# Optimization experiments

Hardware: AMD Instinct MI355X
Metric: run time of the kernel (lower is better)

The kernel has to match this reference:

```python
import jax, jax.numpy as jnp
import numpy as np

DIM = 2048
NUM_HEADS = 16
NUM_KV_HEADS = 4
HEAD_DIM = DIM // NUM_HEADS  # 128
ROPE_DIMS = HEAD_DIM         # rope_dims=0 -> full head_dim
ROPE_BASE = 10000.0
EPS = jnp.finfo(jnp.float32).eps  # torch F.rms_norm default eps


def _rms_norm(x):
    # F.rms_norm over last dim, no learned weight
    return x * jax.lax.rsqrt(jnp.mean(x * x, axis=-1, keepdims=True) + EPS)


def _rope_cos_sin(seq_len, dtype):
    inv_freq = 1.0 / (ROPE_BASE ** (jnp.arange(0, ROPE_DIMS, 2, dtype=jnp.float32) / ROPE_DIMS))
    t = jnp.arange(seq_len, dtype=jnp.float32)
    freqs = jnp.outer(t, inv_freq)  # [S, rope_dims/2]
    return jnp.cos(freqs).astype(dtype), jnp.sin(freqs).astype(dtype)


def _apply_rotary(x, cos, sin):
    # x: [B, H, S, hd]; cos/sin: [S, rope_dims/2] broadcast over B,H
    half = ROPE_DIMS // 2
    x1, x2 = x[..., :half], x[..., half:ROPE_DIMS]
    x_pass = x[..., ROPE_DIMS:]
    rotated = jnp.concatenate((x1 * cos + x2 * sin, -x1 * sin + x2 * cos), axis=-1)
    return jnp.concatenate((rotated, x_pass), axis=-1) if x_pass.shape[-1] else rotated


def setup_inputs() -> dict:
    key = jax.random.key(0)
    ks = jax.random.split(key, 6)
    B, S = 2, 2048
    kv_dim = NUM_KV_HEADS * HEAD_DIM
    scale = 0.02
    return {
        "x": jax.random.normal(ks[0], (B, S, DIM), dtype=jnp.float32),
        "Wq": jax.random.normal(ks[1], (DIM, DIM), dtype=jnp.float32) * scale,
        "Wk": jax.random.normal(ks[2], (kv_dim, DIM), dtype=jnp.float32) * scale,
        "Wv": jax.random.normal(ks[3], (kv_dim, DIM), dtype=jnp.float32) * scale,
        "Wproj": jax.random.normal(ks[4], (DIM, DIM), dtype=jnp.float32) * scale,
        "q_gain": jnp.full((NUM_HEADS,), 1.0, dtype=jnp.float32),
    }


def reference(x, Wq, Wk, Wv, Wproj, q_gain):
    B, S, D = x.shape
    H, KV, hd = NUM_HEADS, NUM_KV_HEADS, HEAD_DIM
    group = H // KV

    # QKV projections (Linear: y = x @ W.T)
    q = (x @ Wq.T).reshape(B, S, H, hd).transpose(0, 2, 1, 3)    # [B,H,S,hd]
    k = (x @ Wk.T).reshape(B, S, KV, hd).transpose(0, 2, 1, 3)   # [B,KV,S,hd]
    v = (x @ Wv.T).reshape(B, S, KV, hd).transpose(0, 2, 1, 3)

    # Per-head RMSNorm on q/k
    q = _rms_norm(q)
    k = _rms_norm(k)

    # RoPE
    cos, sin = _rope_cos_sin(S, q.dtype)
    q = _apply_rotary(q, cos, sin)
    k = _apply_rotary(k, cos, sin)

    # Per-head gain on q
    q = q * q_gain[None, :, None, None]

    # GQA: expand kv heads to H
    k = jnp.repeat(k, group, axis=1)  # [B,H,S,hd]
    v = jnp.repeat(v, group, axis=1)

    # Causal SDPA
    sm_scale = 1.0 / np.sqrt(hd)
    scores = jnp.einsum('bhqd,bhkd->bhqk', q, k) * sm_scale
    causal = jnp.tril(jnp.ones((S, S), dtype=bool))
    scores = jnp.where(causal, scores, -jnp.inf)
    attn = jax.nn.softmax(scores, axis=-1)
    y = jnp.einsum('bhqk,bhkd->bhqd', attn, v)

    y = y.transpose(0, 2, 1, 3).reshape(B, S, D)
    return y @ Wproj.T
```

## Files before the change

kernel.cpp:

```cpp
#include <hip/hip_runtime.h>
#include <hip/hip_bf16.h>
#include <stdint.h>

namespace {

constexpr int kB = 2;
constexpr int kS = 2048;
constexpr int kD = 2048;
constexpr int kH = 16;
constexpr int kKV = 4;
constexpr int kHd = 128;
constexpr int kM = kB * kS;
constexpr int kQKN = kD + kKV * kHd;

using bf = __bf16;
typedef bf bf16x8 __attribute__((ext_vector_type(8)));
typedef float f32x4 __attribute__((ext_vector_type(4)));
typedef float f32x16 __attribute__((ext_vector_type(16)));

__device__ __forceinline__ f32x4 mfma16(bf16x8 a, bf16x8 b, f32x4 c) {
  return __builtin_amdgcn_mfma_f32_16x16x32_bf16(a, b, c, 0, 0, 0);
}
__device__ __forceinline__ f32x16 mfma32(bf16x8 a, bf16x8 b, f32x16 c) {
  return __builtin_amdgcn_mfma_f32_32x32x16_bf16(a, b, c, 0, 0, 0);
}

__device__ __forceinline__ void gload_lds16(const bf* g, bf* l) {
  __builtin_amdgcn_global_load_lds(
      (const __attribute__((address_space(1))) void*)(uintptr_t)g,
      (__attribute__((address_space(3))) void*)l, 16, 0, 0);
}

__global__ __launch_bounds__(256) void cvt_kernel(const float* __restrict__ src,
                                                  bf* __restrict__ dst, int n4) {
  int i = blockIdx.x * 256 + threadIdx.x;
  if (i >= n4) return;
  float4 v = reinterpret_cast<const float4*>(src)[i];
  union { bf h[4]; uint2 u; } o;
  o.h[0] = (bf)v.x; o.h[1] = (bf)v.y; o.h[2] = (bf)v.z; o.h[3] = (bf)v.w;
  reinterpret_cast<uint2*>(dst)[i] = o.u;
}

template <typename CT>
__global__ __launch_bounds__(256) void gemm_bt(const bf* __restrict__ A, int lda,
                                               const bf* __restrict__ Bm, int ldb,
                                               CT* __restrict__ C, int ldc, int K) {
  __shared__ bf As[128 * 64];
  __shared__ bf Bs[128 * 64];
  const int tid = threadIdx.x;
  const int w = tid >> 6, lane = tid & 63;
  const int r16 = lane & 15, kg = lane >> 4;
  const int bm = blockIdx.y * 128, bn = blockIdx.x * 128;
  const int wy = (w >> 1) * 64, wx = (w & 1) * 64;
  f32x4 acc[4][4] = {};
  for (int kt = 0; kt < K; kt += 64) {
    __syncthreads();
#pragma unroll
    for (int r = 0; r < 4; r++) {
      int u = r * 256 + tid;
      int row = u >> 3;
      int cb = ((u & 7) * 16) ^ ((row & 7) << 4);
      gload_lds16(A + (size_t)(bm + row) * lda + kt + (cb >> 1),
                  As + (size_t)(r * 256 + w * 64) * 8);
      gload_lds16(Bm + (size_t)(bn + row) * ldb + kt + (cb >> 1),
                  Bs + (size_t)(r * 256 + w * 64) * 8);
    }
    __syncthreads();
#pragma unroll
    for (int ks = 0; ks < 2; ks++) {
      bf16x8 af[4], bfr[4];
#pragma unroll
      for (int m = 0; m < 4; m++) {
        int row = wy + m * 16 + r16;
        af[m] = *reinterpret_cast<const bf16x8*>(
            reinterpret_cast<const char*>(As) + row * 128 +
            ((ks * 64 + kg * 16) ^ ((row & 7) << 4)));
      }
#pragma unroll
      for (int n = 0; n < 4; n++) {
        int row = wx + n * 16 + r16;
        bfr[n] = *reinterpret_cast<const bf16x8*>(
            reinterpret_cast<const char*>(Bs) + row * 128 +
            ((ks * 64 + kg * 16) ^ ((row & 7) << 4)));
      }
#pragma unroll
      for (int m = 0; m < 4; m++)
#pragma unroll
        for (int n = 0; n < 4; n++)
          acc[m][n] = mfma16(af[m], bfr[n], acc[m][n]);
    }
  }
#pragma unroll
  for (int m = 0; m < 4; m++)
#pragma unroll
    for (int n = 0; n < 4; n++)
#pragma unroll
      for (int r = 0; r < 4; r++) {
        int row = bm + wy + m * 16 + kg * 4 + r;
        int col = bn + wx + n * 16 + r16;
        C[(size_t)row * ldc + col] = (CT)acc[m][n][r];
      }
}

__global__ __launch_bounds__(256) void normrope(bf* __restrict__ qk,
                                                const float* __restrict__ qgain) {
  const int tid = threadIdx.x;
  const int w = tid >> 6, lane = tid & 63;
  int v = blockIdx.x * 4 + w;
  int b = v / (kS * (kH + kKV));
  int rem = v % (kS * (kH + kKV));
  int s = rem / (kH + kKV);
  int j = rem % (kH + kKV);
  int colbase = (j < kH) ? j * kHd : kD + (j - kH) * kHd;
  size_t base = (size_t)(b * kS + s) * kQKN + colbase;
  float e1 = (float)qk[base + lane];
  float e2 = (float)qk[base + 64 + lane];
  float ss = e1 * e1 + e2 * e2;
#pragma unroll
  for (int m = 1; m < 64; m <<= 1) ss += __shfl_xor(ss, m);
  float inv = rsqrtf(ss * (1.0f / 128.0f) + 1.1920929e-7f);
  e1 *= inv; e2 *= inv;
  float invfreq = powf(10000.0f, -(float)lane * (1.0f / 64.0f));
  float ang = (float)s * invfreq;
  float sn, cs;
  sincosf(ang, &sn, &cs);
  float o1 = e1 * cs + e2 * sn;
  float o2 = -e1 * sn + e2 * cs;
  if (j < kH) {
    float g = qgain[j] * (0.08838834764831845f * 1.4426950408889634f);
    o1 *= g; o2 *= g;
  }
  qk[base + lane] = (bf)o1;
  qk[base + 64 + lane] = (bf)o2;
}

__global__ __launch_bounds__(256, 2) void attn_kernel(const bf* __restrict__ qk,
                                                      const bf* __restrict__ vt,
                                                      bf* __restrict__ y) {
  __shared__ bf Ks[2][64 * 128];
  __shared__ bf Vs[2][128 * 64];
  const int tid = threadIdx.x;
  const int w = tid >> 6, lane = tid & 63;
  const int q32 = lane & 31, hi = lane >> 5;
  const int bh = blockIdx.x;
  const int jb = blockIdx.y;
  const int qi = (jb < 8) ? jb : 23 - jb;
  const int b = bh >> 4, h = bh & 15, kvh = h >> 2;
  const size_t rowbase = (size_t)b * kS;
  const bf* kbase = qk + kD + kvh * kHd;
  const bf* vbase = vt + (size_t)(kvh * kHd) * kM + b * kS;

  auto stage = [&](int buf, int kt) {
#pragma unroll
    for (int r = 0; r < 4; r++) {
      int u = r * 256 + tid;
      int krow = u >> 4;
      int cb = ((u & 15) * 16) ^ ((krow & 7) << 4);
      gload_lds16(kbase + (rowbase + kt * 64 + krow) * kQKN + (cb >> 1),
                  Ks[buf] + (size_t)(r * 256 + w * 64) * 8);
    }
#pragma unroll
    for (int r = 0; r < 4; r++) {
      int u = r * 256 + tid;
      int vrow = u >> 3;
      int cb = ((u & 7) * 16) ^ ((vrow & 7) << 4);
      gload_lds16(vbase + (size_t)vrow * kM + kt * 64 + (cb >> 1),
                  Vs[buf] + (size_t)(r * 256 + w * 64) * 8);
    }
  };

  const int q0 = qi * 128;
  const int qg0 = q0 + w * 32;
  const int qrow = qg0 + q32;

  bf16x8 qf[8];
#pragma unroll
  for (int dc = 0; dc < 8; dc++)
    qf[dc] = *reinterpret_cast<const bf16x8*>(
        qk + (rowbase + qrow) * kQKN + h * kHd + dc * 16 + hi * 8);

  f32x16 o[4] = {};
  float mrun = -1e30f, lrun = 0.f;

  int cur = 0;
  stage(0, 0);
  const int ntiles = 2 * qi + 2;

  for (int kt = 0; kt < ntiles; kt++) {
    __syncthreads();
    if (kt + 1 < ntiles) stage(cur ^ 1, kt + 1);

    if (kt * 64 <= qg0 + 31) {
      f32x16 sf[2];
      __builtin_amdgcn_s_setprio(1);
#pragma unroll
      for (int kb = 0; kb < 2; kb++) {
        f32x16 a = {};
#pragma unroll
        for (int dc = 0; dc < 8; dc++) {
          int krow = kb * 32 + q32;
          bf16x8 kf = *reinterpret_cast<const bf16x8*>(
              reinterpret_cast<const char*>(Ks[cur]) + krow * 256 +
              ((dc * 32 + hi * 16) ^ ((krow & 7) << 4)));
          a = mfma32(kf, qf[dc], a);
        }
        sf[kb] = a;
      }
      __builtin_amdgcn_s_setprio(0);

      if (kt * 64 + 63 > qg0) {
#pragma unroll
        for (int kb = 0; kb < 2; kb++)
#pragma unroll
          for (int r = 0; r < 16; r++) {
            int kgl = kt * 64 + kb * 32 + (r & 3) + 8 * (r >> 2) + 4 * hi;
            sf[kb][r] = (kgl <= qrow) ? sf[kb][r] : -1e30f;
          }
      }

      float rmax = sf[0][0];
#pragma unroll
      for (int kb = 0; kb < 2; kb++)
#pragma unroll
        for (int r = 0; r < 16; r++) rmax = fmaxf(rmax, sf[kb][r]);
      rmax = fmaxf(rmax, __shfl_xor(rmax, 32));

      if (!__all(rmax <= mrun + 8.0f)) {
        float mnew = fmaxf(mrun, rmax);
        float resc = exp2f(mrun - mnew);
        mrun = mnew;
        lrun *= resc;
        float rq[16];
#pragma unroll
        for (int r = 0; r < 16; r++)
          rq[r] = __shfl(resc, (r & 3) + 8 * (r >> 2) + 4 * hi);
#pragma unroll
        for (int db = 0; db < 4; db++)
#pragma unroll
          for (int r = 0; r < 16; r++) o[db][r] *= rq[r];
      }

      float rsum = 0.f;
#pragma unroll
      for (int kb = 0; kb < 2; kb++)
#pragma unroll
        for (int r = 0; r < 16; r++) {
          float p = exp2f(sf[kb][r] - mrun);
          sf[kb][r] = p;
          rsum += p;
        }
      rsum += __shfl_xor(rsum, 32);
      lrun += rsum;

      bf16x8 pa[4];
#pragma unroll
      for (int kb = 0; kb < 2; kb++) {
        uint32_t wa[4], wb[4];
#pragma unroll
        for (int g = 0; g < 4; g++) {
          asm("v_cvt_pk_bf16_f32 %0, %1, %2"
              : "=v"(wa[g]) : "v"(sf[kb][4 * g + 0]), "v"(sf[kb][4 * g + 1]));
          asm("v_cvt_pk_bf16_f32 %0, %1, %2"
              : "=v"(wb[g]) : "v"(sf[kb][4 * g + 2]), "v"(sf[kb][4 * g + 3]));
        }
        asm volatile("v_permlane32_swap_b32 %0, %1" : "+v"(wa[0]), "+v"(wa[1]));
        asm volatile("v_permlane32_swap_b32 %0, %1" : "+v"(wb[0]), "+v"(wb[1]));
        asm volatile("v_permlane32_swap_b32 %0, %1" : "+v"(wa[2]), "+v"(wa[3]));
        asm volatile("v_permlane32_swap_b32 %0, %1" : "+v"(wb[2]), "+v"(wb[3]));
        union { uint32_t u[4]; bf16x8 v; } p0, p1;
        p0.u[0] = wa[0]; p0.u[1] = wb[0]; p0.u[2] = wa[1]; p0.u[3] = wb[1];
        p1.u[0] = wa[2]; p1.u[1] = wb[2]; p1.u[2] = wa[3]; p1.u[3] = wb[3];
        pa[2 * kb + 0] = p0.v;
        pa[2 * kb + 1] = p1.v;
      }

      __builtin_amdgcn_s_setprio(1);
#pragma unroll
      for (int c = 0; c < 4; c++)
#pragma unroll
        for (int db = 0; db < 4; db++) {
          int vrow = db * 32 + q32;
          bf16x8 vb = *reinterpret_cast<const bf16x8*>(
              reinterpret_cast<const char*>(Vs[cur]) + vrow * 128 +
              ((c * 32 + hi * 16) ^ ((vrow & 7) << 4)));
          o[db] = mfma32(pa[c], vb, o[db]);
        }
      __builtin_amdgcn_s_setprio(0);
    }
    cur ^= 1;
  }

  float linv = 1.0f / lrun;
  float lq[16];
#pragma unroll
  for (int r = 0; r < 16; r++)
    lq[r] = __shfl(linv, (r & 3) + 8 * (r >> 2) + 4 * hi);
#pragma unroll
  for (int db = 0; db < 4; db++)
#pragma unroll
    for (int r = 0; r < 16; r++) {
      int s = qg0 + (r & 3) + 8 * (r >> 2) + 4 * hi;
      int d = db * 32 + q32;
      y[(rowbase + s) * kD + h * kHd + d] = (bf)(o[db][r] * lq[r]);
    }
}

}

extern "C" void kernel_launch(void* const* d_in, const int* in_sizes, int n_in,
                              void* d_out, int out_size, void* d_ws, size_t ws_size,
                              hipStream_t stream) {
  const float* x  = (const float*)d_in[0];
  const float* Wq = (const float*)d_in[1];
  const float* Wk = (const float*)d_in[2];
  const float* Wv = (const float*)d_in[3];
  const float* Wp = (const float*)d_in[4];
  const float* qg = (const float*)d_in[5];

  bf* xb    = (bf*)d_ws;
  bf* wqkvb = xb + (size_t)kM * kD;
  bf* wpb   = wqkvb + (size_t)3072 * kD;
  bf* qkbuf = wpb + (size_t)kD * kD;
  bf* vtbuf = qkbuf + (size_t)kM * kQKN;
  bf* yb    = vtbuf + (size_t)512 * kM;

  cvt_kernel<<<(kM * kD / 4) / 256, 256, 0, stream>>>(x, xb, kM * kD / 4);
  cvt_kernel<<<(kD * kD / 4) / 256, 256, 0, stream>>>(Wq, wqkvb, kD * kD / 4);
  cvt_kernel<<<(512 * kD / 4) / 256, 256, 0, stream>>>(Wk, wqkvb + (size_t)kD * kD, 512 * kD / 4);
  cvt_kernel<<<(512 * kD / 4) / 256, 256, 0, stream>>>(Wv, wqkvb + (size_t)kD * kD + (size_t)512 * kD, 512 * kD / 4);
  cvt_kernel<<<(kD * kD / 4) / 256, 256, 0, stream>>>(Wp, wpb, kD * kD / 4);

  gemm_bt<bf><<<dim3(kQKN / 128, kM / 128), 256, 0, stream>>>(xb, kD, wqkvb, kD, qkbuf, kQKN, kD);

  gemm_bt<bf><<<dim3(kM / 128, 512 / 128), 256, 0, stream>>>(
      wqkvb + (size_t)(kD + 512) * kD, kD, xb, kD, vtbuf, kM, kD);

  normrope<<<(kB * kS * (kH + kKV)) / 4, 256, 0, stream>>>(qkbuf, qg);

  attn_kernel<<<dim3(kB * kH, 16), 256, 0, stream>>>(qkbuf, vtbuf, yb);

  gemm_bt<float><<<dim3(kD / 128, kM / 128), 256, 0, stream>>>(yb, kD, wpb, kD, (float*)d_out, kD, kD);
}
```

Before: 261.8 us.

## Pair causal query tiles per block and split KV tile across warps

Each attention block now handles two 64-row query tiles, j and 31-j, in sequence, so causal work is balanced across blocks. Within a block, the four warps split as two query halves times two halves of each 64-key tile. The two partial softmax states are then merged through shared memory, reusing the K buffer as scratch. This is meant to remove load imbalance and tail effects from the causal mask, at the cost of half the query reuse per staged K/V tile, an extra LDS merge with syncs per phase, and more redundant tile staging.

```diff
diff --git a/kernel.cpp b/kernel.cpp
--- a/kernel.cpp
+++ b/kernel.cpp
@@ -139,12 +139,13 @@
                                                       bf* __restrict__ y) {
   __shared__ bf Ks[2][64 * 128];
   __shared__ bf Vs[2][128 * 64];
+  __shared__ float Ml[2][64][2];
   const int tid = threadIdx.x;
   const int w = tid >> 6, lane = tid & 63;
   const int q32 = lane & 31, hi = lane >> 5;
+  const int qhalf = w & 1, kvhalf = w >> 1;
   const int bh = blockIdx.x;
-  const int jb = blockIdx.y;
-  const int qi = (jb < 8) ? jb : 23 - jb;
+  const int pairIdx = blockIdx.y;
   const int b = bh >> 4, h = bh & 15, kvh = h >> 2;
   const size_t rowbase = (size_t)b * kS;
   const bf* kbase = qk + kD + kvh * kHd;
@@ -169,140 +170,157 @@
     }
   };
 
-  const int q0 = qi * 128;
-  const int qg0 = q0 + w * 32;
-  const int qrow = qg0 + q32;
-
-  bf16x8 qf[8];
-#pragma unroll
-  for (int dc = 0; dc < 8; dc++)
-    qf[dc] = *reinterpret_cast<const bf16x8*>(
-        qk + (rowbase + qrow) * kQKN + h * kHd + dc * 16 + hi * 8);
-
-  f32x16 o[4] = {};
-  float mrun = -1e30f, lrun = 0.f;
-
-  int cur = 0;
-  stage(0, 0);
-  const int ntiles = 2 * qi + 2;
-
-  for (int kt = 0; kt < ntiles; kt++) {
-    __syncthreads();
-    if (kt + 1 < ntiles) stage(cur ^ 1, kt + 1);
-
-    if (kt * 64 <= qg0 + 31) {
-      f32x16 sf[2];
-      __builtin_amdgcn_s_setprio(1);
-#pragma unroll
-      for (int kb = 0; kb < 2; kb++) {
-        f32x16 a = {};
+#pragma unroll 1
+  for (int ph = 0; ph < 2; ph++) {
+    const int j = ph ? (31 - pairIdx) : pairIdx;
+    const int q0 = j * 64;
+    const int qg0 = q0 + qhalf * 32;
+    const int qrow = qg0 + q32;
+    const int kvoff = kvhalf * 32;
+
+    bf16x8 qf[8];
+#pragma unroll
+    for (int dc = 0; dc < 8; dc++)
+      qf[dc] = *reinterpret_cast<const bf16x8*>(
+          qk + (rowbase + qrow) * kQKN + h * kHd + dc * 16 + hi * 8);
+
+    f32x16 o[4] = {};
+    float mrun = -1e30f, lrun = 0.f;
+
+    int cur = 0;
+    stage(0, 0);
+
+    for (int kt = 0; kt <= j; kt++) {
+      __syncthreads();
+      if (kt < j) stage(cur ^ 1, kt + 1);
+
+      if (kt * 64 + kvoff <= qg0 + 31) {
+        f32x16 sf = {};
+        __builtin_amdgcn_s_setprio(1);
 #pragma unroll
         for (int dc = 0; dc < 8; dc++) {
-          int krow = kb * 32 + q32;
+          int krow = kvoff + q32;
           bf16x8 kf = *reinterpret_cast<const bf16x8*>(
               reinterpret_cast<const char*>(Ks[cur]) + krow * 256 +
               ((dc * 32 + hi * 16) ^ ((krow & 7) << 4)));
-          a = mfma32(kf, qf[dc], a);
-        }
-        sf[kb] = a;
-      }
-      __builtin_amdgcn_s_setprio(0);
-
-      if (kt * 64 + 63 > qg0) {
-#pragma unroll
-        for (int kb = 0; kb < 2; kb++)
+          sf = mfma32(kf, qf[dc], sf);
+        }
+        __builtin_amdgcn_s_setprio(0);
+
+        if (kt * 64 + kvoff + 31 > qg0) {
 #pragma unroll
           for (int r = 0; r < 16; r++) {
-            int kgl = kt * 64 + kb * 32 + (r & 3) + 8 * (r >> 2) + 4 * hi;
-            sf[kb][r] = (kgl <= qrow) ? sf[kb][r] : -1e30f;
+            int kgl = kt * 64 + kvoff + (r & 3) + 8 * (r >> 2) + 4 * hi;
+            sf[r] = (kgl <= qrow) ? sf[r] : -1e30f;
           }
-      }
-
-      float rmax = sf[0][0];
-#pragma unroll
-      for (int kb = 0; kb < 2; kb++)
-#pragma unroll
-        for (int r = 0; r < 16; r++) rmax = fmaxf(rmax, sf[kb][r]);
-      rmax = fmaxf(rmax, __shfl_xor(rmax, 32));
-
-      if (!__all(rmax <= mrun + 8.0f)) {
-        float mnew = fmaxf(mrun, rmax);
-        float resc = exp2f(mrun - mnew);
-        mrun = mnew;
-        lrun *= resc;
-        float rq[16];
+        }
+
+        float rmax = sf[0];
+#pragma unroll
+        for (int r = 1; r < 16; r++) rmax = fmaxf(rmax, sf[r]);
+        rmax = fmaxf(rmax, __shfl_xor(rmax, 32));
+
+        if (!__all(rmax <= mrun + 8.0f)) {
+          float mnew = fmaxf(mrun, rmax);
+          float resc = exp2f(mrun - mnew);
+          mrun = mnew;
+          lrun *= resc;
+          float rq[16];
+#pragma unroll
+          for (int r = 0; r < 16; r++)
+            rq[r] = __shfl(resc, (r & 3) + 8 * (r >> 2) + 4 * hi);
+#pragma unroll
+          for (int db = 0; db < 4; db++)
+#pragma unroll
+            for (int r = 0; r < 16; r++) o[db][r] *= rq[r];
+        }
+
+        float rsum = 0.f;
+#pragma unroll
+        for (int r = 0; r < 16; r++) {
+          float p = exp2f(sf[r] - mrun);
+          sf[r] = p;
+          rsum += p;
+        }
+        rsum += __shfl_xor(rsum, 32);
+        lrun += rsum;
+
+        bf16x8 pa[2];
+        {
+          uint32_t wa[4], wb[4];
+#pragma unroll
+          for (int g = 0; g < 4; g++) {
+            asm("v_cvt_pk_bf16_f32 %0, %1, %2"
+                : "=v"(wa[g]) : "v"(sf[4 * g + 0]), "v"(sf[4 * g + 1]));
+            asm("v_cvt_pk_bf16_f32 %0, %1, %2"
+                : "=v"(wb[g]) : "v"(sf[4 * g + 2]), "v"(sf[4 * g + 3]));
+          }
+          asm volatile("v_permlane32_swap_b32 %0, %1" : "+v"(wa[0]), "+v"(wa[1]));
+          asm volatile("v_permlane32_swap_b32 %0, %1" : "+v"(wb[0]), "+v"(wb[1]));
+          asm volatile("v_permlane32_swap_b32 %0, %1" : "+v"(wa[2]), "+v"(wa[3]));
+          asm volatile("v_permlane32_swap_b32 %0, %1" : "+v"(wb[2]), "+v"(wb[3]));
+          union { uint32_t u[4]; bf16x8 v; } p0, p1;
+          p0.u[0] = wa[0]; p0.u[1] = wb[0]; p0.u[2] = wa[1]; p0.u[3] = wb[1];
+          p1.u[0] = wa[2]; p1.u[1] = wb[2]; p1.u[2] = wa[3]; p1.u[3] = wb[3];
+          pa[0] = p0.v; pa[1] = p1.v;
+        }
+
+        __builtin_amdgcn_s_setprio(1);
+#pragma unroll
+        for (int c = 0; c < 2; c++)
+#pragma unroll
+          for (int db = 0; db < 4; db++) {
+            int vrow = db * 32 + q32;
+            bf16x8 vb = *reinterpret_cast<const bf16x8*>(
+                reinterpret_cast<const char*>(Vs[cur]) + vrow * 128 +
+                ((kvhalf * 64 + c * 32 + hi * 16) ^ ((vrow & 7) << 4)));
+            o[db] = mfma32(pa[c], vb, o[db]);
+          }
+        __builtin_amdgcn_s_setprio(0);
+      }
+      cur ^= 1;
+    }
+
+    __syncthreads();
+    float* mb = reinterpret_cast<float*>(Ks);
+    if (w >= 2) {
+      Ml[w - 2][lane][0] = mrun;
+      Ml[w - 2][lane][1] = lrun;
+      int base = (w - 2) * 4096;
+#pragma unroll
+      for (int db = 0; db < 4; db++)
 #pragma unroll
         for (int r = 0; r < 16; r++)
-          rq[r] = __shfl(resc, (r & 3) + 8 * (r >> 2) + 4 * hi);
-#pragma unroll
-        for (int db = 0; db < 4; db++)
-#pragma unroll
-          for (int r = 0; r < 16; r++) o[db][r] *= rq[r];
-      }
-
-      float rsum = 0.f;
-#pragma unroll
-      for (int kb = 0; kb < 2; kb++)
+          mb[base + (db * 16 + r) * 64 + lane] = o[db][r];
+    }
+    __syncthreads();
+    if (w < 2) {
+      float m1 = Ml[w][lane][0], l1 = Ml[w][lane][1];
+      float m = fmaxf(mrun, m1);
+      float f0 = exp2f(mrun - m), f1 = exp2f(m1 - m);
+      float linv = 1.0f / (lrun * f0 + l1 * f1);
+      float av = f0 * linv, bv = f1 * linv;
+      float aq[16], bq[16];
+#pragma unroll
+      for (int r = 0; r < 16; r++) {
+        int cr = (r & 3) + 8 * (r >> 2) + 4 * hi;
+        aq[r] = __shfl(av, cr);
+        bq[r] = __shfl(bv, cr);
+      }
+      int base = w * 4096;
+#pragma unroll
+      for (int db = 0; db < 4; db++)
 #pragma unroll
         for (int r = 0; r < 16; r++) {
-          float p = exp2f(sf[kb][r] - mrun);
-          sf[kb][r] = p;
-          rsum += p;
-        }
-      rsum += __shfl_xor(rsum, 32);
-      lrun += rsum;
-
-      bf16x8 pa[4];
-#pragma unroll
-      for (int kb = 0; kb < 2; kb++) {
-        uint32_t wa[4], wb[4];
-#pragma unroll
-        for (int g = 0; g < 4; g++) {
-          asm("v_cvt_pk_bf16_f32 %0, %1, %2"
-              : "=v"(wa[g]) : "v"(sf[kb][4 * g + 0]), "v"(sf[kb][4 * g + 1]));
-          asm("v_cvt_pk_bf16_f32 %0, %1, %2"
-              : "=v"(wb[g]) : "v"(sf[kb][4 * g + 2]), "v"(sf[kb][4 * g + 3]));
-        }
-        asm volatile("v_permlane32_swap_b32 %0, %1" : "+v"(wa[0]), "+v"(wa[1]));
-        asm volatile("v_permlane32_swap_b32 %0, %1" : "+v"(wb[0]), "+v"(wb[1]));
-        asm volatile("v_permlane32_swap_b32 %0, %1" : "+v"(wa[2]), "+v"(wa[3]));
-        asm volatile("v_permlane32_swap_b32 %0, %1" : "+v"(wb[2]), "+v"(wb[3]));
-        union { uint32_t u[4]; bf16x8 v; } p0, p1;
-        p0.u[0] = wa[0]; p0.u[1] = wb[0]; p0.u[2] = wa[1]; p0.u[3] = wb[1];
-        p1.u[0] = wa[2]; p1.u[1] = wb[2]; p1.u[2] = wa[3]; p1.u[3] = wb[3];
-        pa[2 * kb + 0] = p0.v;
-        pa[2 * kb + 1] = p1.v;
-      }
-
-      __builtin_amdgcn_s_setprio(1);
-#pragma unroll
-      for (int c = 0; c < 4; c++)
-#pragma unroll
-        for (int db = 0; db < 4; db++) {
-          int vrow = db * 32 + q32;
-          bf16x8 vb = *reinterpret_cast<const bf16x8*>(
-              reinterpret_cast<const char*>(Vs[cur]) + vrow * 128 +
-              ((c * 32 + hi * 16) ^ ((vrow & 7) << 4)));
-          o[db] = mfma32(pa[c], vb, o[db]);
-        }
-      __builtin_amdgcn_s_setprio(0);
-    }
-    cur ^= 1;
+          float pv = mb[base + (db * 16 + r) * 64 + lane];
+          float res = o[db][r] * aq[r] + pv * bq[r];
+          int s = qg0 + (r & 3) + 8 * (r >> 2) + 4 * hi;
+          int d = db * 32 + q32;
+          y[(rowbase + s) * kD + h * kHd + d] = (bf)res;
+        }
+    }
+    __syncthreads();
   }
-
-  float linv = 1.0f / lrun;
-  float lq[16];
-#pragma unroll
-  for (int r = 0; r < 16; r++)
-    lq[r] = __shfl(linv, (r & 3) + 8 * (r >> 2) + 4 * hi);
-#pragma unroll
-  for (int db = 0; db < 4; db++)
-#pragma unroll
-    for (int r = 0; r < 16; r++) {
-      int s = qg0 + (r & 3) + 8 * (r >> 2) + 4 * hi;
-      int d = db * 32 + q32;
-      y[(rowbase + s) * kD + h * kHd + d] = (bf)(o[db][r] * lq[r]);
-    }
 }
 
 }
```

Measured after the change: 251.3 us. 1.04x faster.
